# Kernel tuning notes

Measured on AMD Instinct MI355X. Metric: run time of the kernel, lower is better.

Reference implementation:

```python
import jax, jax.numpy as jnp
import numpy as np

N_NODES = 50000
N_EDGES = 1_600_000
D_IN, D_HID, D_OUT = 512, 256, 64


def setup_inputs() -> dict:
    key = jax.random.key(0)
    ks = jax.random.split(key, 8)
    x = jax.random.normal(ks[0], (N_NODES, D_IN), dtype=jnp.float32)
    edge_rows = jax.random.randint(ks[1], (N_EDGES,), 0, N_NODES, dtype=jnp.int32)
    edge_cols = jax.random.randint(ks[2], (N_EDGES,), 0, N_NODES, dtype=jnp.int32)
    # normalized adjacency values (e.g. D^-1/2 A D^-1/2 entries)
    edge_vals = jax.random.uniform(ks[3], (N_EDGES,), dtype=jnp.float32)
    W1 = jax.random.normal(ks[4], (D_IN, D_HID), dtype=jnp.float32) * (1.0 / np.sqrt(D_IN))
    b1 = jnp.zeros((D_HID,), dtype=jnp.float32)
    W2 = jax.random.normal(ks[5], (D_HID, D_OUT), dtype=jnp.float32) * (1.0 / np.sqrt(D_HID))
    b2 = jnp.zeros((D_OUT,), dtype=jnp.float32)
    return {"x": x, "edge_rows": edge_rows, "edge_cols": edge_cols,
            "edge_vals": edge_vals, "W1": W1, "b1": b1, "W2": W2, "b2": b2}


def _spmm(rows, cols, vals, h):
    # out[r] = sum_{e: rows[e]==r} vals[e] * h[cols[e]]
    msgs = vals[:, None] * h[cols]          # [E, d] gather
    return jax.ops.segment_sum(msgs, rows, num_segments=N_NODES)


def reference(x, edge_rows, edge_cols, edge_vals, W1, b1, W2, b2):
    h = x @ W1 + b1                          # W1(x)
    h = _spmm(edge_rows, edge_cols, edge_vals, h)  # sparse.mm(A_hat, h)
    h = jax.nn.relu(h)                       # relu; dropout is identity in eval
    h = h @ W2 + b2                           # W2(h)
    out = _spmm(edge_rows, edge_cols, edge_vals, h)
    return out
```

## Files before the change

kernel.cpp:

```cpp
#include <hip/hip_runtime.h>
#include <hip/hip_bf16.h>

constexpr int NN = 50000;
constexpr int NE = 1600000;
constexpr int DI = 512;
constexpr int DH = 256;
constexpr int DO = 64;

constexpr int NC = NN * 16;
constexpr int G1_BLOCKS = ((NN + 127) / 128) * (DH / 128);
constexpr int SC_BLOCKS = 2048;
constexpr int SCAN_BLOCKS = (NN + 1023) / 1024;
constexpr int E4_CAP = NE + NN * 16 + 64;

typedef __attribute__((ext_vector_type(8))) short short8;
typedef __attribute__((ext_vector_type(4))) float f32x4;

__device__ inline ushort f2b(float f) {
    uint u = __float_as_uint(f);
    u += 0x7fffu + ((u >> 16) & 1u);
    return (ushort)(u >> 16);
}
__device__ inline float b2f(ushort u) {
    return __uint_as_float((uint)u << 16);
}
__device__ inline void gload16(const void* g, void* l) {
    __builtin_amdgcn_global_load_lds(
        (const __attribute__((address_space(1))) unsigned int*)g,
        (__attribute__((address_space(3))) unsigned int*)l, 16, 0, 0);
}


__global__ void k_prep(const float* __restrict__ X, ushort* __restrict__ Xb,
                       const float* __restrict__ W1, ushort* __restrict__ w1bT,
                       const int* __restrict__ er, const int* __restrict__ ec,
                       int* __restrict__ counts2, uint* __restrict__ rc32) {
    const int bid = blockIdx.x;
    const int tid = threadIdx.x;
    if (bid < 1024) {
        const float4* x4 = (const float4*)X;
        ushort4* o4 = (ushort4*)Xb;
        const int stride = 1024 * 256;
        for (int i = bid * 256 + tid; i < NN * DI / 4; i += stride) {
            float4 v = x4[i];
            o4[i] = make_ushort4(f2b(v.x), f2b(v.y), f2b(v.z), f2b(v.w));
        }
        for (int i = bid * 256 + tid; i < DI * DH; i += stride) {
            int n = i >> 9, k = i & 511;
            w1bT[i] = f2b(W1[(size_t)k * DH + n]);
        }
    } else {
        const int4* r4 = (const int4*)er;
        const int4* c4 = (const int4*)ec;
        const int stride = 1024 * 256;
        for (int i = (bid - 1024) * 256 + tid; i < NE / 4; i += stride) {
            int4 r = r4[i];
            int4 c = c4[i];
            *(uint4*)&rc32[i * 4] = make_uint4(
                ((uint)r.x << 16) | (uint)c.x, ((uint)r.y << 16) | (uint)c.y,
                ((uint)r.z << 16) | (uint)c.z, ((uint)r.w << 16) | (uint)c.w);
            atomicAdd(&counts2[(r.x << 4) | (c.x >> 12)], 1);
            atomicAdd(&counts2[(r.y << 4) | (c.y >> 12)], 1);
            atomicAdd(&counts2[(r.z << 4) | (c.z >> 12)], 1);
            atomicAdd(&counts2[(r.w << 4) | (c.w >> 12)], 1);
        }
    }
}


__global__ __launch_bounds__(1024) void k_scanA(const int* __restrict__ counts2,
                                                int* __restrict__ rp,
                                                int* __restrict__ partials) {
    const int t = threadIdx.x;
    const int r = blockIdx.x * 1024 + t;
    int s = 0;
    if (r < NN) {
        const int4* c4 = (const int4*)(counts2 + (size_t)r * 16);
        int4 a = c4[0], b = c4[1], c = c4[2], d = c4[3];
        s = a.x + a.y + a.z + a.w + b.x + b.y + b.z + b.w
          + c.x + c.y + c.z + c.w + d.x + d.y + d.z + d.w;
        s = (s + 15) & ~15;
    }
    __shared__ int buf[1024];
    buf[t] = s;
    __syncthreads();
    for (int off = 1; off < 1024; off <<= 1) {
        int v = (t >= off) ? buf[t - off] : 0;
        __syncthreads();
        buf[t] += v;
        __syncthreads();
    }
    if (r < NN) rp[r] = buf[t] - s;
    if (t == 1023) partials[blockIdx.x] = buf[1023];
}

__global__ __launch_bounds__(64) void k_scanB(int* __restrict__ partials,
                                              int* __restrict__ rp) {
    __shared__ int buf[64];
    int t = threadIdx.x;
    int v = (t < SCAN_BLOCKS) ? partials[t] : 0;
    buf[t] = v;
    __syncthreads();
    for (int off = 1; off < 64; off <<= 1) {
        int x = (t >= off) ? buf[t - off] : 0;
        __syncthreads();
        buf[t] += x;
        __syncthreads();
    }
    if (t < SCAN_BLOCKS) partials[t] = buf[t] - v;
    if (t == 63) rp[NN] = buf[63];
}

__global__ __launch_bounds__(1024) void k_scanC(const int* __restrict__ counts2,
                                                int* __restrict__ rp,
                                                int* __restrict__ cur2,
                                                const int* __restrict__ partials,
                                                const float* __restrict__ W2,
                                                ushort* __restrict__ w2bT) {
    const int t = threadIdx.x;
    const int r = blockIdx.x * 1024 + t;
    if (r < NN) {
        const int off = partials[blockIdx.x];
        const int base = rp[r] + off;
        rp[r] = base;
        const int4* c4 = (const int4*)(counts2 + (size_t)r * 16);
        int4 ca = c4[0], cb = c4[1], cc = c4[2], cd = c4[3];
        int cnt[16] = {ca.x, ca.y, ca.z, ca.w, cb.x, cb.y, cb.z, cb.w,
                       cc.x, cc.y, cc.z, cc.w, cd.x, cd.y, cd.z, cd.w};
        int out[16];
        int rs = 0;
        #pragma unroll
        for (int b = 0; b < 16; ++b) { out[b] = base + rs; rs += cnt[b]; }
        int4* o4 = (int4*)(cur2 + (size_t)r * 16);
        o4[0] = make_int4(out[0],  out[1],  out[2],  out[3]);
        o4[1] = make_int4(out[4],  out[5],  out[6],  out[7]);
        o4[2] = make_int4(out[8],  out[9],  out[10], out[11]);
        o4[3] = make_int4(out[12], out[13], out[14], out[15]);
    }
    if (blockIdx.x == 0) {
        for (int i = t; i < DH * DO; i += 1024) {
            int n = i >> 8, k = i & 255;
            w2bT[i] = f2b(W2[(size_t)k * DO + n]);
        }
    }
}


__global__ __launch_bounds__(256, 4) void k_gemm1(const ushort* __restrict__ Xb,
                                                  const ushort* __restrict__ w1bT,
                                                  const float* __restrict__ B,
                                                  ushort* __restrict__ H) {
    __shared__ ushort As[128 * 32];
    __shared__ ushort Bs[128 * 32];
    const int bid = blockIdx.x;
    const int bm = (bid >> 1) * 128;
    const int bn = (bid & 1) * 128;
    const int tid = threadIdx.x;
    const int wid = tid >> 6, lane = tid & 63;
    const int wm = wid >> 1, wn = wid & 1;
    const int lr = lane & 15, lg = lane >> 4;

    f32x4 acc[4][4];
    #pragma unroll
    for (int i = 0; i < 4; ++i)
        #pragma unroll
        for (int j = 0; j < 4; ++j)
            acc[i][j] = (f32x4){0.f, 0.f, 0.f, 0.f};

    for (int kt = 0; kt < DI; kt += 32) {
        #pragma unroll
        for (int c = 0; c < 2; ++c) {
            int i = c * 256 + tid;
            int row = i >> 2, slot = i & 3;
            const ushort* g = Xb + (size_t)(bm + row) * DI + kt + slot * 8;
            gload16(g, As + (size_t)(c * 256 + wid * 64) * 8);
        }
        #pragma unroll
        for (int c = 0; c < 2; ++c) {
            int i = c * 256 + tid;
            int row = i >> 2, slot = i & 3;
            const ushort* g = w1bT + (size_t)(bn + row) * DI + kt + slot * 8;
            gload16(g, Bs + (size_t)(c * 256 + wid * 64) * 8);
        }
        __syncthreads();

        short8 a[4], b[4];
        #pragma unroll
        for (int f = 0; f < 4; ++f) {
            a[f] = *(short8*)&As[(wm * 64 + f * 16 + lr) * 32 + lg * 8];
            b[f] = *(short8*)&Bs[(wn * 64 + f * 16 + lr) * 32 + lg * 8];
        }
        #pragma unroll
        for (int i = 0; i < 4; ++i)
            #pragma unroll
            for (int j = 0; j < 4; ++j)
                acc[i][j] = __builtin_amdgcn_mfma_f32_16x16x32_bf16(a[i], b[j], acc[i][j], 0, 0, 0);
        __syncthreads();
    }

    #pragma unroll
    for (int i = 0; i < 4; ++i) {
        int r0 = bm + wm * 64 + i * 16 + lg * 4;
        #pragma unroll
        for (int j = 0; j < 4; ++j) {
            int col = bn + wn * 64 + j * 16 + lr;
            float bias = B[col];
            #pragma unroll
            for (int e = 0; e < 4; ++e) {
                int r = r0 + e;
                if (r < NN) H[(size_t)r * DH + col] = f2b(acc[i][j][e] + bias);
            }
        }
    }
}


__global__ __launch_bounds__(256) void k_scatter(const uint* __restrict__ rc32,
                                                 const float* __restrict__ ev,
                                                 int* __restrict__ cur2,
                                                 uint* __restrict__ e4) {
    const int g = blockIdx.x & 7;
    const uint lo = g * (NN / 8), hi = lo + (NN / 8);
    const uint4* rc4 = (const uint4*)rc32;
    for (int q = (blockIdx.x >> 3) * 256 + (int)threadIdx.x; q < NE / 4;
         q += (SC_BLOCKS / 8) * 256) {
        uint4 t = rc4[q];
        #pragma unroll
        for (int e = 0; e < 4; ++e) {
            uint rc = (e == 0) ? t.x : (e == 1) ? t.y : (e == 2) ? t.z : t.w;
            uint rr = rc >> 16;
            if (rr >= lo && rr < hi) {
                uint c = rc & 0xffffu;
                float v = ev[q * 4 + e];
                int p = atomicAdd(&cur2[(rr << 4) | (c >> 12)], 1);
                e4[p] = c | ((uint)f2b(v) << 16);
            }
        }
    }
}


__global__ __launch_bounds__(256) void k_srg(const int* __restrict__ rp,
                                             const uint* __restrict__ e4,
                                             const ushort* __restrict__ H,
                                             const ushort* __restrict__ w2bT,
                                             const float* __restrict__ B2,
                                             ushort* __restrict__ H2) {
    __shared__ ushort hs[16][264];
    const int tid = threadIdx.x;
    const int w = tid >> 6, lane = tid & 63;
    const int half = lane >> 5;
    const int dl = lane & 31;
    const ushort* gbase = H + dl * 8;
    const uint4* eq = (const uint4*)e4;

    #pragma unroll
    for (int q = 0; q < 4; ++q) {
        const int r = blockIdx.x * 16 + w * 4 + q;
        const int s = rp[r], e = rp[r + 1];
        float a[8] = {0.f, 0.f, 0.f, 0.f, 0.f, 0.f, 0.f, 0.f};

        int qi = s >> 2;
        uint4 q0 = eq[qi], q1 = eq[qi + 1], q2 = eq[qi + 2], q3 = eq[qi + 3];
        for (int i = s; i < e; i += 16) {
            uint u[8];
            u[0] = half ? q0.y : q0.x;  u[1] = half ? q0.w : q0.z;
            u[2] = half ? q1.y : q1.x;  u[3] = half ? q1.w : q1.z;
            u[4] = half ? q2.y : q2.x;  u[5] = half ? q2.w : q2.z;
            u[6] = half ? q3.y : q3.x;  u[7] = half ? q3.w : q3.z;
            uint4 hw[8];
            #pragma unroll
            for (int k = 0; k < 8; ++k)
                hw[k] = *(const uint4*)(gbase + (size_t)(u[k] & 0xffffu) * DH);
            qi += 4;
            q0 = eq[qi]; q1 = eq[qi + 1]; q2 = eq[qi + 2]; q3 = eq[qi + 3];
            #pragma unroll
            for (int k = 0; k < 8; ++k) {
                float v = __uint_as_float(u[k] & 0xffff0000u);
                uint w0 = hw[k].x, w1 = hw[k].y, w2 = hw[k].z, w3 = hw[k].w;
                a[0] += v * __uint_as_float(w0 << 16);
                a[1] += v * __uint_as_float(w0 & 0xffff0000u);
                a[2] += v * __uint_as_float(w1 << 16);
                a[3] += v * __uint_as_float(w1 & 0xffff0000u);
                a[4] += v * __uint_as_float(w2 << 16);
                a[5] += v * __uint_as_float(w2 & 0xffff0000u);
                a[6] += v * __uint_as_float(w3 << 16);
                a[7] += v * __uint_as_float(w3 & 0xffff0000u);
            }
        }
        #pragma unroll
        for (int d = 0; d < 8; ++d) a[d] += __shfl_xor(a[d], 32);
        if (half == 0) {
            short8 o;
            #pragma unroll
            for (int d = 0; d < 8; ++d) o[d] = (short)f2b(fmaxf(a[d], 0.f));
            *(short8*)&hs[w * 4 + q][dl * 8] = o;
        }
    }
    __syncthreads();

    const int lr = lane & 15, lg = lane >> 4;
    f32x4 acc = (f32x4){0.f, 0.f, 0.f, 0.f};
    #pragma unroll
    for (int kt = 0; kt < DH; kt += 32) {
        short8 af = *(short8*)&hs[lr][kt + lg * 8];
        short8 bf = *(const short8*)(w2bT + (size_t)(w * 16 + lr) * DH + kt + lg * 8);
        acc = __builtin_amdgcn_mfma_f32_16x16x32_bf16(af, bf, acc, 0, 0, 0);
    }
    const int col = w * 16 + lr;
    const float bias = B2[col];
    #pragma unroll
    for (int e = 0; e < 4; ++e) {
        int row = blockIdx.x * 16 + lg * 4 + e;
        H2[(size_t)row * DO + col] = f2b(acc[e] + bias);
    }
}


__global__ __launch_bounds__(256) void k_spmm_out(const int* __restrict__ rp,
                                                  const uint* __restrict__ e4,
                                                  const ushort* __restrict__ H2,
                                                  float* __restrict__ OUT) {
    const int r = blockIdx.x * 4 + (threadIdx.x >> 6);
    const int lane = threadIdx.x & 63;
    const int slot = lane >> 3;
    const int dq = lane & 7;
    const int s = rp[r], e = rp[r + 1];
    const ushort* base = H2 + dq * 8;
    float a[8] = {0.f, 0.f, 0.f, 0.f, 0.f, 0.f, 0.f, 0.f};

    for (int i = s; i < e; i += 16) {
        uint2 u = *(const uint2*)(e4 + i + 2 * slot);
        short8 h0 = *(const short8*)(base + (size_t)(u.x & 0xffffu) * DO);
        short8 h1 = *(const short8*)(base + (size_t)(u.y & 0xffffu) * DO);
        float v0 = __uint_as_float(u.x & 0xffff0000u);
        float v1 = __uint_as_float(u.y & 0xffff0000u);
        #pragma unroll
        for (int d = 0; d < 8; ++d)
            a[d] += v0 * b2f((ushort)h0[d]) + v1 * b2f((ushort)h1[d]);
    }
    #pragma unroll
    for (int d = 0; d < 8; ++d) {
        a[d] += __shfl_xor(a[d], 8);
        a[d] += __shfl_xor(a[d], 16);
        a[d] += __shfl_xor(a[d], 32);
    }
    if (slot == 0) {
        float* o = OUT + (size_t)r * DO + dq * 8;
        *(float4*)o       = make_float4(a[0], a[1], a[2], a[3]);
        *(float4*)(o + 4) = make_float4(a[4], a[5], a[6], a[7]);
    }
}


extern "C" void kernel_launch(void* const* d_in, const int* in_sizes, int n_in,
                              void* d_out, int out_size, void* d_ws, size_t ws_size,
                              hipStream_t stream) {
    const float* x  = (const float*)d_in[0];
    const int*   er = (const int*)d_in[1];
    const int*   ec = (const int*)d_in[2];
    const float* ev = (const float*)d_in[3];
    const float* W1 = (const float*)d_in[4];
    const float* b1 = (const float*)d_in[5];
    const float* W2 = (const float*)d_in[6];
    const float* b2 = (const float*)d_in[7];
    float* out = (float*)d_out;

    char* ws = (char*)d_ws;
    ushort* Xb  = (ushort*)ws;
    uint*   e4  = (uint*)ws;
    ws += (size_t)NN * DI * 2;
    ushort* h1  = (ushort*)ws; ws += (size_t)NN * DH * 2;
    ushort* h2  = (ushort*)ws;
    uint*   rc32 = (uint*)ws;  ws += (size_t)NN * DO * 2;
    int* counts2 = (int*)ws;   ws += ((size_t)NC * 4 + 255) & ~(size_t)255;
    int* rp     = (int*)ws;    ws += ((size_t)(NN + 1) * 4 + 255) & ~(size_t)255;
    int* cur2   = (int*)ws;    ws += ((size_t)NC * 4 + 255) & ~(size_t)255;
    int* partials = (int*)ws;  ws += 256;
    ushort* w1bT = (ushort*)ws; ws += ((size_t)DI * DH * 2 + 255) & ~(size_t)255;
    ushort* w2bT = (ushort*)ws; ws += ((size_t)DH * DO * 2 + 255) & ~(size_t)255;

    hipMemsetAsync(counts2, 0, (size_t)NC * 4, stream);
    k_prep<<<2048, 256, 0, stream>>>(x, Xb, W1, w1bT, er, ec, counts2, rc32);
    k_scanA<<<SCAN_BLOCKS, 1024, 0, stream>>>(counts2, rp, partials);
    k_scanB<<<1, 64, 0, stream>>>(partials, rp);
    k_scanC<<<SCAN_BLOCKS, 1024, 0, stream>>>(counts2, rp, cur2, partials, W2, w2bT);
    k_gemm1<<<G1_BLOCKS, 256, 0, stream>>>(Xb, w1bT, b1, h1);
    hipMemsetAsync(e4, 0, (size_t)E4_CAP * 4, stream);
    k_scatter<<<SC_BLOCKS, 256, 0, stream>>>(rc32, ev, cur2, e4);
    k_srg<<<NN / 16, 256, 0, stream>>>(rp, e4, h1, w2bT, b2, h2);
    k_spmm_out<<<NN / 4, 256, 0, stream>>>(rp, e4, h2, out);
}
```

Baseline: 328.5 us.

## Swizzle GEMM1 LDS tiles, pre-convert edge values to bf16, rebalance prep work

The GEMM1 shared-memory tiles get an XOR swizzle on the 16-byte slot index, applied both to the global-to-LDS load addresses and to the fragment reads, to reduce LDS bank conflicts. Edge values are converted to bf16 once in the prep kernel's edge half. The scatter pass, which runs eight filtered sweeps over all edges, then reads 2-byte values instead of 4-byte floats. The W1 and W2 transposes move into the lighter edge-processing blocks of k_prep, which also removes the W2 work from scanC, at the cost of an extra workspace buffer.

Result: no change. 322.7 us (-1.8%).

```diff
diff --git a/kernel.cpp b/kernel.cpp
--- a/kernel.cpp
+++ b/kernel.cpp
@@ -33,8 +33,11 @@
 
 __global__ void k_prep(const float* __restrict__ X, ushort* __restrict__ Xb,
                        const float* __restrict__ W1, ushort* __restrict__ w1bT,
+                       const float* __restrict__ W2, ushort* __restrict__ w2bT,
                        const int* __restrict__ er, const int* __restrict__ ec,
-                       int* __restrict__ counts2, uint* __restrict__ rc32) {
+                       const float* __restrict__ ev,
+                       int* __restrict__ counts2, uint* __restrict__ rc32,
+                       ushort* __restrict__ evb) {
     const int bid = blockIdx.x;
     const int tid = threadIdx.x;
     if (bid < 1024) {
@@ -45,24 +48,33 @@
             float4 v = x4[i];
             o4[i] = make_ushort4(f2b(v.x), f2b(v.y), f2b(v.z), f2b(v.w));
         }
-        for (int i = bid * 256 + tid; i < DI * DH; i += stride) {
-            int n = i >> 9, k = i & 511;
-            w1bT[i] = f2b(W1[(size_t)k * DH + n]);
-        }
     } else {
+        const int b = bid - 1024;
+        const int stride = 1024 * 256;
         const int4* r4 = (const int4*)er;
         const int4* c4 = (const int4*)ec;
-        const int stride = 1024 * 256;
-        for (int i = (bid - 1024) * 256 + tid; i < NE / 4; i += stride) {
+        const float4* v4 = (const float4*)ev;
+        for (int i = b * 256 + tid; i < NE / 4; i += stride) {
             int4 r = r4[i];
             int4 c = c4[i];
+            float4 v = v4[i];
             *(uint4*)&rc32[i * 4] = make_uint4(
                 ((uint)r.x << 16) | (uint)c.x, ((uint)r.y << 16) | (uint)c.y,
                 ((uint)r.z << 16) | (uint)c.z, ((uint)r.w << 16) | (uint)c.w);
+            *(ushort4*)&evb[i * 4] =
+                make_ushort4(f2b(v.x), f2b(v.y), f2b(v.z), f2b(v.w));
             atomicAdd(&counts2[(r.x << 4) | (c.x >> 12)], 1);
             atomicAdd(&counts2[(r.y << 4) | (c.y >> 12)], 1);
             atomicAdd(&counts2[(r.z << 4) | (c.z >> 12)], 1);
             atomicAdd(&counts2[(r.w << 4) | (c.w >> 12)], 1);
+        }
+        for (int i = b * 256 + tid; i < DI * DH; i += stride) {
+            int n = i >> 9, k = i & 511;
+            w1bT[i] = f2b(W1[(size_t)k * DH + n]);
+        }
+        for (int i = b * 256 + tid; i < DH * DO; i += stride) {
+            int n = i >> 8, k = i & 255;
+            w2bT[i] = f2b(W2[(size_t)k * DO + n]);
         }
     }
 }
@@ -114,9 +126,7 @@
 __global__ __launch_bounds__(1024) void k_scanC(const int* __restrict__ counts2,
                                                 int* __restrict__ rp,
                                                 int* __restrict__ cur2,
-                                                const int* __restrict__ partials,
-                                                const float* __restrict__ W2,
-                                                ushort* __restrict__ w2bT) {
+                                                const int* __restrict__ partials) {
     const int t = threadIdx.x;
     const int r = blockIdx.x * 1024 + t;
     if (r < NN) {
@@ -136,12 +146,6 @@
         o4[1] = make_int4(out[4],  out[5],  out[6],  out[7]);
         o4[2] = make_int4(out[8],  out[9],  out[10], out[11]);
         o4[3] = make_int4(out[12], out[13], out[14], out[15]);
-    }
-    if (blockIdx.x == 0) {
-        for (int i = t; i < DH * DO; i += 1024) {
-            int n = i >> 8, k = i & 255;
-            w2bT[i] = f2b(W2[(size_t)k * DO + n]);
-        }
     }
 }
 
@@ -159,6 +163,7 @@
     const int wid = tid >> 6, lane = tid & 63;
     const int wm = wid >> 1, wn = wid & 1;
     const int lr = lane & 15, lg = lane >> 4;
+    const int swz = (lg ^ (lr & 3)) * 8;
 
     f32x4 acc[4][4];
     #pragma unroll
@@ -172,14 +177,16 @@
         for (int c = 0; c < 2; ++c) {
             int i = c * 256 + tid;
             int row = i >> 2, slot = i & 3;
-            const ushort* g = Xb + (size_t)(bm + row) * DI + kt + slot * 8;
+            int ss = slot ^ (row & 3);
+            const ushort* g = Xb + (size_t)(bm + row) * DI + kt + ss * 8;
             gload16(g, As + (size_t)(c * 256 + wid * 64) * 8);
         }
         #pragma unroll
         for (int c = 0; c < 2; ++c) {
             int i = c * 256 + tid;
             int row = i >> 2, slot = i & 3;
-            const ushort* g = w1bT + (size_t)(bn + row) * DI + kt + slot * 8;
+            int ss = slot ^ (row & 3);
+            const ushort* g = w1bT + (size_t)(bn + row) * DI + kt + ss * 8;
             gload16(g, Bs + (size_t)(c * 256 + wid * 64) * 8);
         }
         __syncthreads();
@@ -187,8 +194,8 @@
         short8 a[4], b[4];
         #pragma unroll
         for (int f = 0; f < 4; ++f) {
-            a[f] = *(short8*)&As[(wm * 64 + f * 16 + lr) * 32 + lg * 8];
-            b[f] = *(short8*)&Bs[(wn * 64 + f * 16 + lr) * 32 + lg * 8];
+            a[f] = *(short8*)&As[(wm * 64 + f * 16 + lr) * 32 + swz];
+            b[f] = *(short8*)&Bs[(wn * 64 + f * 16 + lr) * 32 + swz];
         }
         #pragma unroll
         for (int i = 0; i < 4; ++i)
@@ -216,7 +223,7 @@
 
 
 __global__ __launch_bounds__(256) void k_scatter(const uint* __restrict__ rc32,
-                                                 const float* __restrict__ ev,
+                                                 const ushort* __restrict__ evb,
                                                  int* __restrict__ cur2,
                                                  uint* __restrict__ e4) {
     const int g = blockIdx.x & 7;
@@ -231,9 +238,9 @@
             uint rr = rc >> 16;
             if (rr >= lo && rr < hi) {
                 uint c = rc & 0xffffu;
-                float v = ev[q * 4 + e];
+                uint vb = evb[q * 4 + e];
                 int p = atomicAdd(&cur2[(rr << 4) | (c >> 12)], 1);
-                e4[p] = c | ((uint)f2b(v) << 16);
+                e4[p] = c | (vb << 16);
             }
         }
     }
@@ -379,15 +386,17 @@
     int* partials = (int*)ws;  ws += 256;
     ushort* w1bT = (ushort*)ws; ws += ((size_t)DI * DH * 2 + 255) & ~(size_t)255;
     ushort* w2bT = (ushort*)ws; ws += ((size_t)DH * DO * 2 + 255) & ~(size_t)255;
+    ushort* evb  = (ushort*)ws; ws += ((size_t)NE * 2 + 255) & ~(size_t)255;
 
     hipMemsetAsync(counts2, 0, (size_t)NC * 4, stream);
-    k_prep<<<2048, 256, 0, stream>>>(x, Xb, W1, w1bT, er, ec, counts2, rc32);
+    k_prep<<<2048, 256, 0, stream>>>(x, Xb, W1, w1bT, W2, w2bT,
+                                     er, ec, ev, counts2, rc32, evb);
     k_scanA<<<SCAN_BLOCKS, 1024, 0, stream>>>(counts2, rp, partials);
     k_scanB<<<1, 64, 0, stream>>>(partials, rp);
-    k_scanC<<<SCAN_BLOCKS, 1024, 0, stream>>>(counts2, rp, cur2, partials, W2, w2bT);
+    k_scanC<<<SCAN_BLOCKS, 1024, 0, stream>>>(counts2, rp, cur2, partials);
     k_gemm1<<<G1_BLOCKS, 256, 0, stream>>>(Xb, w1bT, b1, h1);
     hipMemsetAsync(e4, 0, (size_t)E4_CAP * 4, stream);
-    k_scatter<<<SC_BLOCKS, 256, 0, stream>>>(rc32, ev, cur2, e4);
+    k_scatter<<<SC_BLOCKS, 256, 0, stream>>>(rc32, evb, cur2, e4);
     k_srg<<<NN / 16, 256, 0, stream>>>(rp, e4, h1, w2bT, b2, h2);
     k_spmm_out<<<NN / 4, 256, 0, stream>>>(rp, e4, h2, out);
 }
```
